# Kernel optimization log

Hardware: AMD Instinct MI355X
Metric: run time of the kernel (lower is better)

Reference implementation:

```python
import jax, jax.numpy as jnp
import numpy as np

B, L, D_MODEL = 4, 2048, 256
D_STATE, D_CONV, EXPAND = 16, 4, 2
D_INNER = EXPAND * D_MODEL          # 512
DT_RANK = (D_MODEL + 15) // 16      # 16
HORIZON = 96


def setup_inputs() -> dict:
    key = jax.random.key(0)
    ks = jax.random.split(key, 8)
    s = lambda k, shape, scale=0.02: jax.random.normal(k, shape, dtype=jnp.float32) * scale
    return {
        "x": jax.random.normal(ks[0], (B, L, D_MODEL), dtype=jnp.float32),
        "in_proj_w": s(ks[1], (2 * D_INNER, D_MODEL)),          # no bias (mamba default)
        "conv_w": s(ks[2], (D_INNER, 1, D_CONV), 0.1),          # depthwise causal conv
        "conv_b": jnp.zeros((D_INNER,), jnp.float32),
        "x_proj_w": s(ks[3], (DT_RANK + 2 * D_STATE, D_INNER)),
        "dt_proj_w": s(ks[4], (D_INNER, DT_RANK), 0.1),
        # softplus^{-1}(0.01): typical small initial dt
        "dt_proj_b": jnp.log(jnp.expm1(jnp.full((D_INNER,), 0.01, jnp.float32))),
        "A_log": jnp.log(jnp.broadcast_to(jnp.arange(1, D_STATE + 1, dtype=jnp.float32), (D_INNER, D_STATE))),
        "D_param": jnp.ones((D_INNER,), jnp.float32),
        "out_proj_w": s(ks[5], (D_MODEL, D_INNER)),
        "head_w": s(ks[6], (HORIZON, D_MODEL)),
        "head_b": jnp.zeros((HORIZON,), jnp.float32),
    }


def _silu(x):
    return x * jax.nn.sigmoid(x)


def _forward(x, in_proj_w, conv_w, conv_b, x_proj_w, dt_proj_w, dt_proj_b,
             A_log, D_param, out_proj_w, head_w, head_b):
    # in_proj -> split into conv/ssm branch and gate z
    xz = x @ in_proj_w.T                      # (B, L, 2*d_inner)
    x_in, z = jnp.split(xz, 2, axis=-1)
    # depthwise causal conv over time
    x_t = jnp.transpose(x_in, (0, 2, 1))      # (B, d_inner, L)
    x_conv = jax.lax.conv_general_dilated(
        x_t, conv_w, (1,), [(D_CONV - 1, 0)],
        feature_group_count=D_INNER, dimension_numbers=("NCH", "OIH", "NCH"))
    u = _silu(jnp.transpose(x_conv + conv_b[None, :, None], (0, 2, 1)))  # (B, L, d_inner)
    # input-dependent dt, B, C
    x_dbl = u @ x_proj_w.T
    dt, Bm, Cm = jnp.split(x_dbl, [DT_RANK, DT_RANK + D_STATE], axis=-1)
    delta = jax.nn.softplus(dt @ dt_proj_w.T + dt_proj_b)  # (B, L, d_inner)
    A = -jnp.exp(A_log)                                     # (d_inner, d_state)
    deltaA = jnp.exp(delta[..., None] * A)                  # (B, L, d_inner, d_state)
    deltaBu = delta[..., None] * Bm[:, :, None, :] * u[..., None]

    def step(h, ins):
        dA, dBu, c = ins                                    # (B,d,n),(B,d,n),(B,n)
        h = dA * h + dBu
        y = jnp.einsum("bdn,bn->bd", h, c)
        return h, y

    h0 = jnp.zeros((x.shape[0], D_INNER, D_STATE), x.dtype)
    xs = (jnp.moveaxis(deltaA, 1, 0), jnp.moveaxis(deltaBu, 1, 0), jnp.moveaxis(Cm, 1, 0))
    _, ys = jax.lax.scan(step, h0, xs)                      # (L, B, d_inner)
    y = jnp.moveaxis(ys, 0, 1) + u * D_param
    y = y * _silu(z)
    out = y @ out_proj_w.T                                  # (B, L, d_model)
    last = out[:, -1, :]
    return last @ head_w.T + head_b                         # (B, HORIZON)


def reference(x, in_proj_w, conv_w, conv_b, x_proj_w, dt_proj_w, dt_proj_b,
              A_log, D_param, out_proj_w, head_w, head_b):
    return _forward(x, in_proj_w, conv_w, conv_b, x_proj_w, dt_proj_w, dt_proj_b,
                    A_log, D_param, out_proj_w, head_w, head_b)
```

## Files before the change

kernel.cpp:

```cpp
#include <hip/hip_runtime.h>
#include <math.h>

#define BATCH 4
#define LSEQ 2048
#define BL (BATCH*LSEQ)
#define DMODEL 256
#define DINNER 512
#define NSTATE 16
#define DTRANK 16
#define NPROJ 48
#define HORIZ 96
#define NCH 32
#define TCH (LSEQ/NCH)
#define PSTRIDE (BL*NPROJ)

typedef __attribute__((ext_vector_type(8))) short short8b;
typedef __attribute__((ext_vector_type(4))) float f32x4;

__device__ __forceinline__ unsigned short f2bf(float f) {
  unsigned u = __float_as_uint(f);
  u += 0x7FFF + ((u >> 16) & 1);
  return (unsigned short)(u >> 16);
}

__global__ __launch_bounds__(512) void k_front(const float* __restrict__ X,
                                               const float* __restrict__ W,
                                               const float* __restrict__ cw,
                                               const float* __restrict__ cb,
                                               const float* __restrict__ xpw,
                                               const float* __restrict__ opw,
                                               const float* __restrict__ hw,
                                               float* __restrict__ uT,
                                               float* __restrict__ part,
                                               float* __restrict__ hwf) {
  __shared__ unsigned short sBX[48 * 264];
  __shared__ float sw2[48 * 132];
  __shared__ float u_lds[128 * 36];
  const int tid = threadIdx.x;
  const int bx = blockIdx.x;
  if (bx >= 512) {
    const int fid = bx - 512;
    const int k0 = fid * 8;
    float* scratch = u_lds;
    {
      int m = tid >> 1;
      int half = (tid & 1) << 2;
      *(float4*)&scratch[m * 8 + half] =
        *(const float4*)&opw[(size_t)m * DINNER + k0 + half];
    }
    __syncthreads();
    for (int u = tid; u < HORIZ * 8; u += 512) {
      int t = u >> 3, kk = u & 7;
      const float* hr = &hw[(size_t)t * DMODEL];
      float acc = 0.f;
      #pragma unroll 8
      for (int m = 0; m < DMODEL; ++m) acc = fmaf(hr[m], scratch[m*8 + kk], acc);
      hwf[(size_t)t * DINNER + k0 + kk] = acc;
    }
    return;
  }
  const int btc = bx >> 1;
  const int jp  = bx & 1;
  const int bt0 = btc * 32;
  const bool edge0 = ((bt0 & (LSEQ - 1)) == 0);
  const int lane = tid & 63;
  const int w  = tid >> 6;
  const int fl = lane & 15;
  const int fg = lane >> 4;
  for (int u = tid; u < 1536; u += 512) {
    int tok = u >> 5, ko = u & 31;
    int g = bt0 - 16 + tok;
    if (g < 0) g = 0;
    const float* xr = &X[(size_t)g * DMODEL + ko * 8];
    float4 a = *(const float4*)xr, b = *(const float4*)(xr + 4);
    unsigned short t8[8] = {f2bf(a.x), f2bf(a.y), f2bf(a.z), f2bf(a.w),
                            f2bf(b.x), f2bf(b.y), f2bf(b.z), f2bf(b.w)};
    *(short8b*)&sBX[tok * 264 + ko * 8] = *(short8b*)t8;
  }
  const int sj = tid >> 2;
  const int sk = tid & 3;
  const int tf = w & 1;
  const int of = w >> 1;
  f32x4 xacc = {0.f, 0.f, 0.f, 0.f};
  for (int jc = 0; jc < 2; ++jc) {
    const int jbase = jp * 256 + jc * 128;
    __syncthreads();
    for (int u = tid; u < 1536; u += 512) {
      int o = u >> 5, k4 = (u & 31) << 2;
      *(float4*)&sw2[o * 132 + k4] = *(const float4*)&xpw[(size_t)o * DINNER + jbase + k4];
    }
    short8b aw[8];
    {
      const float* wrow = &W[(size_t)(jbase + w * 16 + fl) * DMODEL + fg * 8];
      #pragma unroll
      for (int ks = 0; ks < 8; ++ks) {
        float4 a = *(const float4*)(wrow + ks * 32);
        float4 b = *(const float4*)(wrow + ks * 32 + 4);
        unsigned short t8[8] = {f2bf(a.x), f2bf(a.y), f2bf(a.z), f2bf(a.w),
                                f2bf(b.x), f2bf(b.y), f2bf(b.z), f2bf(b.w)};
        aw[ks] = *(short8b*)t8;
      }
    }
    f32x4 acc0 = {0,0,0,0}, acc1 = {0,0,0,0}, acc2 = {0,0,0,0};
    #pragma unroll
    for (int ks = 0; ks < 8; ++ks) {
      const int kcol = (ks * 4 + fg) * 8;
      short8b x0 = *(short8b*)&sBX[(fl)      * 264 + kcol];
      short8b x1 = *(short8b*)&sBX[(16 + fl) * 264 + kcol];
      short8b x2 = *(short8b*)&sBX[(32 + fl) * 264 + kcol];
      acc0 = __builtin_amdgcn_mfma_f32_16x16x32_bf16(x0, aw[ks], acc0, 0, 0, 0);
      acc1 = __builtin_amdgcn_mfma_f32_16x16x32_bf16(x1, aw[ks], acc1, 0, 0, 0);
      acc2 = __builtin_amdgcn_mfma_f32_16x16x32_bf16(x2, aw[ks], acc2, 0, 0, 0);
    }
    if (edge0) acc0 = (f32x4){0,0,0,0};
    const int j = jbase + w * 16 + fl;
    const float4 cwv = *(const float4*)&cw[j * 4];
    const float cbv = cb[j];
    float u1[4], u2[4];
    {
      float s3a = __shfl(acc1[3], lane - 16), s3b = __shfl(acc0[3], lane + 48);
      float s2a = __shfl(acc1[2], lane - 16), s2b = __shfl(acc0[2], lane + 48);
      float s1a = __shfl(acc1[1], lane - 16), s1b = __shfl(acc0[1], lane + 48);
      float p1 = fg ? s3a : s3b, p2 = fg ? s2a : s2b, p3 = fg ? s1a : s1b;
      float xm1[4] = {p1, acc1[0], acc1[1], acc1[2]};
      float xm2[4] = {p2, p1, acc1[0], acc1[1]};
      float xm3[4] = {p3, p2, p1, acc1[0]};
      #pragma unroll
      for (int r = 0; r < 4; ++r) {
        float s = cbv;
        s = fmaf(cwv.x, xm3[r], s); s = fmaf(cwv.y, xm2[r], s);
        s = fmaf(cwv.z, xm1[r], s); s = fmaf(cwv.w, acc1[r], s);
        u1[r] = s / (1.f + __expf(-s));
      }
    }
    {
      float s3a = __shfl(acc2[3], lane - 16), s3b = __shfl(acc1[3], lane + 48);
      float s2a = __shfl(acc2[2], lane - 16), s2b = __shfl(acc1[2], lane + 48);
      float s1a = __shfl(acc2[1], lane - 16), s1b = __shfl(acc1[1], lane + 48);
      float p1 = fg ? s3a : s3b, p2 = fg ? s2a : s2b, p3 = fg ? s1a : s1b;
      float xm1[4] = {p1, acc2[0], acc2[1], acc2[2]};
      float xm2[4] = {p2, p1, acc2[0], acc2[1]};
      float xm3[4] = {p3, p2, p1, acc2[0]};
      #pragma unroll
      for (int r = 0; r < 4; ++r) {
        float s = cbv;
        s = fmaf(cwv.x, xm3[r], s); s = fmaf(cwv.y, xm2[r], s);
        s = fmaf(cwv.z, xm1[r], s); s = fmaf(cwv.w, acc2[r], s);
        u2[r] = s / (1.f + __expf(-s));
      }
    }
    {
      const int jl = w * 16 + fl;
      #pragma unroll
      for (int r = 0; r < 4; ++r) {
        u_lds[jl * 36 + fg * 4 + r]      = u1[r];
        u_lds[jl * 36 + 16 + fg * 4 + r] = u2[r];
      }
    }
    __syncthreads();
    {
      const int tq = sk * 8;
      float4 a = *(float4*)&u_lds[sj * 36 + tq];
      float4 b = *(float4*)&u_lds[sj * 36 + tq + 4];
      *(float4*)&uT[(size_t)(jbase + sj) * BL + bt0 + tq]     = a;
      *(float4*)&uT[(size_t)(jbase + sj) * BL + bt0 + tq + 4] = b;
    }
    if (w < 6) {
      #pragma unroll
      for (int s = 0; s < 4; ++s) {
        unsigned short ua[8];
        #pragma unroll
        for (int e = 0; e < 8; ++e)
          ua[e] = f2bf(u_lds[(s * 32 + fg * 8 + e) * 36 + tf * 16 + fl]);
        const float* wr = &sw2[(of * 16 + fl) * 132 + s * 32 + fg * 8];
        float4 w0 = *(const float4*)wr, w1 = *(const float4*)(wr + 4);
        unsigned short wb[8] = {f2bf(w0.x), f2bf(w0.y), f2bf(w0.z), f2bf(w0.w),
                                f2bf(w1.x), f2bf(w1.y), f2bf(w1.z), f2bf(w1.w)};
        xacc = __builtin_amdgcn_mfma_f32_16x16x32_bf16(*(short8b*)ua, *(short8b*)wb,
                                                       xacc, 0, 0, 0);
      }
    }
  }
  if (w < 6) {
    float4 v = make_float4(xacc[0], xacc[1], xacc[2], xacc[3]);
    *(float4*)&part[(size_t)jp * PSTRIDE +
                    (size_t)(bt0 + tf * 16 + fl) * NPROJ + of * 16 + fg * 4] = v;
  }
}

__global__ __launch_bounds__(256) void k_scan(const float* __restrict__ uT,
                                              const float* __restrict__ part,
                                              const float* __restrict__ dtw,
                                              const float* __restrict__ dtb,
                                              const float* __restrict__ Alog,
                                              float* __restrict__ aprod,
                                              float* __restrict__ hacc) {
  __shared__ float sdt[64][17];
  __shared__ float sB[64][16];
  __shared__ float sdp[16][66][2];
  __shared__ float su[16][68];
  __shared__ float sdtw[16][17];
  __shared__ float sdtb[16];
  const int dblk = blockIdx.x, c = blockIdx.y, b = blockIdx.z;
  const int tid = threadIdx.x;
  const int d0 = dblk * 16;
  const int bt0 = b * LSEQ + c * TCH;
  {
    int tok = tid >> 2, q = (tid & 3) << 2;
    size_t base = (size_t)(bt0 + tok) * NPROJ + q;
    float4 v0 = *(const float4*)&part[base];
    float4 v1 = *(const float4*)&part[base + PSTRIDE];
    sdt[tok][q] = v0.x + v1.x; sdt[tok][q + 1] = v0.y + v1.y;
    sdt[tok][q + 2] = v0.z + v1.z; sdt[tok][q + 3] = v0.w + v1.w;
    float4 w0 = *(const float4*)&part[base + DTRANK];
    float4 w1 = *(const float4*)&part[base + DTRANK + PSTRIDE];
    float4 ww = make_float4(w0.x + w1.x, w0.y + w1.y, w0.z + w1.z, w0.w + w1.w);
    *(float4*)&sB[tok][q] = ww;
    int dl = tid >> 4, tq = (tid & 15) << 2;
    *(float4*)&su[dl][tq] = *(const float4*)&uT[(size_t)(d0 + dl) * BL + bt0 + tq];
    sdtw[tid >> 4][tid & 15] = dtw[(d0 + (tid >> 4)) * DTRANK + (tid & 15)];
    if (tid < 16) sdtb[tid] = dtb[d0 + tid];
  }
  __syncthreads();
  {
    int tok = tid >> 2, dl4 = (tid & 3) << 2;
    #pragma unroll
    for (int dd = 0; dd < 4; ++dd) {
      int dl = dl4 + dd;
      float a = sdtb[dl];
      #pragma unroll
      for (int r = 0; r < DTRANK; ++r) a = fmaf(sdt[tok][r], sdtw[dl][r], a);
      float dlt = (a > 20.f) ? a : log1pf(__expf(a));
      sdp[dl][tok][0] = dlt;
      sdp[dl][tok][1] = dlt * su[dl][tok];
    }
  }
  __syncthreads();
  const int dl = tid >> 4, n = tid & 15;
  const int d = d0 + dl;
  const float A = -__expf(Alog[d * NSTATE + n]);
  float ap = 1.f, h = 0.f;
  #pragma unroll 8
  for (int tt = 0; tt < TCH; ++tt) {
    float2 dp = *(const float2*)&sdp[dl][tt][0];
    float dA = __expf(dp.x * A);
    h = fmaf(dA, h, dp.y * sB[tt][n]);
    ap *= dA;
  }
  size_t off = (((size_t)b * NCH + c) * DINNER + d) * NSTATE + n;
  aprod[off] = ap;
  hacc[off] = h;
}

__global__ __launch_bounds__(256) void k_combine(const float* __restrict__ aprod,
                                                 const float* __restrict__ hacc,
                                                 const float* __restrict__ part,
                                                 const float* __restrict__ uT,
                                                 const float* __restrict__ Dp,
                                                 const float* __restrict__ X,
                                                 const float* __restrict__ ipw,
                                                 float* __restrict__ ybuf) {
  __shared__ float sx[DMODEL];
  const int dblk = blockIdx.x & 31, b = blockIdx.x >> 5;
  const int tid = threadIdx.x;
  const int dl = tid >> 4, n = tid & 15;
  const int d = dblk * 16 + dl;
  sx[tid] = X[((size_t)b * LSEQ + LSEQ - 1) * DMODEL + tid];
  float h = 0.f;
  for (int c = 0; c < NCH; ++c) {
    size_t off = (((size_t)b * NCH + c) * DINNER + d) * NSTATE + n;
    h = fmaf(aprod[off], h, hacc[off]);
  }
  __syncthreads();
  float zp = 0.f;
  {
    const float* zr = &ipw[(size_t)(DINNER + d) * DMODEL + (n << 4)];
    #pragma unroll
    for (int q = 0; q < 4; ++q) {
      float4 w4 = *(const float4*)&zr[q << 2];
      float4 x4 = *(const float4*)&sx[(n << 4) + (q << 2)];
      zp = fmaf(w4.x, x4.x, zp); zp = fmaf(w4.y, x4.y, zp);
      zp = fmaf(w4.z, x4.z, zp); zp = fmaf(w4.w, x4.w, zp);
    }
  }
  const int btL = b * LSEQ + LSEQ - 1;
  size_t cbase = (size_t)btL * NPROJ + DTRANK + NSTATE + n;
  float Cv = part[cbase] + part[cbase + PSTRIDE];
  float v = h * Cv;
  #pragma unroll
  for (int off = 1; off < 16; off <<= 1) {
    v  += __shfl_xor(v, off);
    zp += __shfl_xor(zp, off);
  }
  if (n == 0) {
    float y = v + uT[(size_t)d * BL + btL] * Dp[d];
    ybuf[b * DINNER + d] = y * zp / (1.f + __expf(-zp));
  }
}

__global__ __launch_bounds__(256) void k_out(const float* __restrict__ sy,
                                             const float* __restrict__ hwf,
                                             const float* __restrict__ hb,
                                             float* __restrict__ out) {
  const int t = blockIdx.x;
  const int b = threadIdx.x >> 6;
  const int lane = threadIdx.x & 63;
  const int k0 = lane << 3;
  const float* yr = &sy[(size_t)b * DINNER + k0];
  const float* wr = &hwf[(size_t)t * DINNER + k0];
  float4 y0 = *(const float4*)yr, y1 = *(const float4*)(yr + 4);
  float4 w0 = *(const float4*)wr, w1 = *(const float4*)(wr + 4);
  float s = y0.x * w0.x + y0.y * w0.y + y0.z * w0.z + y0.w * w0.w
          + y1.x * w1.x + y1.y * w1.y + y1.z * w1.z + y1.w * w1.w;
  #pragma unroll
  for (int off = 1; off < 64; off <<= 1) s += __shfl_xor(s, off);
  if (lane == 0) out[b * HORIZ + t] = s + hb[t];
}

extern "C" void kernel_launch(void* const* d_in, const int* in_sizes, int n_in,
                              void* d_out, int out_size, void* d_ws, size_t ws_size,
                              hipStream_t stream) {
  (void)in_sizes; (void)n_in; (void)out_size; (void)ws_size;
  const float* x    = (const float*)d_in[0];
  const float* ipw  = (const float*)d_in[1];
  const float* cw   = (const float*)d_in[2];
  const float* cb   = (const float*)d_in[3];
  const float* xpw  = (const float*)d_in[4];
  const float* dtw  = (const float*)d_in[5];
  const float* dtb  = (const float*)d_in[6];
  const float* Alog = (const float*)d_in[7];
  const float* Dp   = (const float*)d_in[8];
  const float* opw  = (const float*)d_in[9];
  const float* hw   = (const float*)d_in[10];
  const float* hb   = (const float*)d_in[11];
  float* out = (float*)d_out;
  float* ws  = (float*)d_ws;

  float* uT    = ws;
  float* part  = ws + 4194304;
  float* aprod = ws + 4980736;
  float* hacc  = ws + 6029312;
  float* ybuf  = ws + 7077888;
  float* hwf   = ws + 7079936;

  k_front<<<576, 512, 0, stream>>>(x, ipw, cw, cb, xpw, opw, hw, uT, part, hwf);
  k_scan<<<dim3(32, NCH, BATCH), 256, 0, stream>>>(uT, part, dtw, dtb, Alog, aprod, hacc);
  k_combine<<<128, 256, 0, stream>>>(aprod, hacc, part, uT, Dp, x, ipw, ybuf);
  k_out<<<HORIZ, 256, 0, stream>>>(ybuf, hwf, hb, out);
}
```

Before: 74.37 us.

## Store intermediate u activations in bf16 and pre-convert x_proj weights in LDS

New measurement: 72.55 us (median of 3 runs). -2.4%, faster.

```diff
diff --git a/kernel.cpp b/kernel.cpp
--- a/kernel.cpp
+++ b/kernel.cpp
@@ -15,12 +15,16 @@
 #define PSTRIDE (BL*NPROJ)
 
 typedef __attribute__((ext_vector_type(8))) short short8b;
+typedef __attribute__((ext_vector_type(4))) short short4b;
 typedef __attribute__((ext_vector_type(4))) float f32x4;
 
 __device__ __forceinline__ unsigned short f2bf(float f) {
   unsigned u = __float_as_uint(f);
   u += 0x7FFF + ((u >> 16) & 1);
   return (unsigned short)(u >> 16);
+}
+__device__ __forceinline__ float bf2f(unsigned short h) {
+  return __uint_as_float(((unsigned)h) << 16);
 }
 
 __global__ __launch_bounds__(512) void k_front(const float* __restrict__ X,
@@ -30,18 +34,18 @@
                                                const float* __restrict__ xpw,
                                                const float* __restrict__ opw,
                                                const float* __restrict__ hw,
-                                               float* __restrict__ uT,
+                                               unsigned short* __restrict__ uTb,
                                                float* __restrict__ part,
                                                float* __restrict__ hwf) {
   __shared__ unsigned short sBX[48 * 264];
-  __shared__ float sw2[48 * 132];
-  __shared__ float u_lds[128 * 36];
+  __shared__ unsigned short sw2b[48 * 136];
+  __shared__ unsigned short u_ldsb[128 * 40];
   const int tid = threadIdx.x;
   const int bx = blockIdx.x;
   if (bx >= 512) {
     const int fid = bx - 512;
     const int k0 = fid * 8;
-    float* scratch = u_lds;
+    float* scratch = (float*)sBX;
     {
       int m = tid >> 1;
       int half = (tid & 1) << 2;
@@ -59,8 +63,8 @@
     }
     return;
   }
-  const int btc = bx >> 1;
-  const int jp  = bx & 1;
+  const int btc = bx & 255;
+  const int jp  = bx >> 8;
   const int bt0 = btc * 32;
   const bool edge0 = ((bt0 & (LSEQ - 1)) == 0);
   const int lane = tid & 63;
@@ -85,9 +89,13 @@
   for (int jc = 0; jc < 2; ++jc) {
     const int jbase = jp * 256 + jc * 128;
     __syncthreads();
-    for (int u = tid; u < 1536; u += 512) {
-      int o = u >> 5, k4 = (u & 31) << 2;
-      *(float4*)&sw2[o * 132 + k4] = *(const float4*)&xpw[(size_t)o * DINNER + jbase + k4];
+    for (int u = tid; u < 768; u += 512) {
+      int o = u >> 4, k8 = (u & 15) * 8;
+      const float* src = &xpw[(size_t)o * DINNER + jbase + k8];
+      float4 a = *(const float4*)src, b = *(const float4*)(src + 4);
+      unsigned short t8[8] = {f2bf(a.x), f2bf(a.y), f2bf(a.z), f2bf(a.w),
+                              f2bf(b.x), f2bf(b.y), f2bf(b.z), f2bf(b.w)};
+      *(short8b*)&sw2b[o * 136 + k8] = *(short8b*)t8;
     }
     short8b aw[8];
     {
@@ -151,19 +159,16 @@
     }
     {
       const int jl = w * 16 + fl;
-      #pragma unroll
-      for (int r = 0; r < 4; ++r) {
-        u_lds[jl * 36 + fg * 4 + r]      = u1[r];
-        u_lds[jl * 36 + 16 + fg * 4 + r] = u2[r];
-      }
+      unsigned short b1[4] = {f2bf(u1[0]), f2bf(u1[1]), f2bf(u1[2]), f2bf(u1[3])};
+      unsigned short b2[4] = {f2bf(u2[0]), f2bf(u2[1]), f2bf(u2[2]), f2bf(u2[3])};
+      *(short4b*)&u_ldsb[jl * 40 + fg * 4]      = *(short4b*)b1;
+      *(short4b*)&u_ldsb[jl * 40 + 16 + fg * 4] = *(short4b*)b2;
     }
     __syncthreads();
     {
       const int tq = sk * 8;
-      float4 a = *(float4*)&u_lds[sj * 36 + tq];
-      float4 b = *(float4*)&u_lds[sj * 36 + tq + 4];
-      *(float4*)&uT[(size_t)(jbase + sj) * BL + bt0 + tq]     = a;
-      *(float4*)&uT[(size_t)(jbase + sj) * BL + bt0 + tq + 4] = b;
+      *(short8b*)&uTb[(size_t)(jbase + sj) * BL + bt0 + tq] =
+        *(short8b*)&u_ldsb[sj * 40 + tq];
     }
     if (w < 6) {
       #pragma unroll
@@ -171,12 +176,9 @@
         unsigned short ua[8];
         #pragma unroll
         for (int e = 0; e < 8; ++e)
-          ua[e] = f2bf(u_lds[(s * 32 + fg * 8 + e) * 36 + tf * 16 + fl]);
-        const float* wr = &sw2[(of * 16 + fl) * 132 + s * 32 + fg * 8];
-        float4 w0 = *(const float4*)wr, w1 = *(const float4*)(wr + 4);
-        unsigned short wb[8] = {f2bf(w0.x), f2bf(w0.y), f2bf(w0.z), f2bf(w0.w),
-                                f2bf(w1.x), f2bf(w1.y), f2bf(w1.z), f2bf(w1.w)};
-        xacc = __builtin_amdgcn_mfma_f32_16x16x32_bf16(*(short8b*)ua, *(short8b*)wb,
+          ua[e] = u_ldsb[(s * 32 + fg * 8 + e) * 40 + tf * 16 + fl];
+        short8b wb = *(short8b*)&sw2b[(of * 16 + fl) * 136 + s * 32 + fg * 8];
+        xacc = __builtin_amdgcn_mfma_f32_16x16x32_bf16(*(short8b*)ua, wb,
                                                        xacc, 0, 0, 0);
       }
     }
@@ -188,7 +190,7 @@
   }
 }
 
-__global__ __launch_bounds__(256) void k_scan(const float* __restrict__ uT,
+__global__ __launch_bounds__(256) void k_scan(const unsigned short* __restrict__ uTb,
                                               const float* __restrict__ part,
                                               const float* __restrict__ dtw,
                                               const float* __restrict__ dtb,
@@ -216,8 +218,12 @@
     float4 w1 = *(const float4*)&part[base + DTRANK + PSTRIDE];
     float4 ww = make_float4(w0.x + w1.x, w0.y + w1.y, w0.z + w1.z, w0.w + w1.w);
     *(float4*)&sB[tok][q] = ww;
-    int dl = tid >> 4, tq = (tid & 15) << 2;
-    *(float4*)&su[dl][tq] = *(const float4*)&uT[(size_t)(d0 + dl) * BL + bt0 + tq];
+    int dl = tid >> 4, t4 = (tid & 15) << 2;
+    short4b uv = *(const short4b*)&uTb[(size_t)(d0 + dl) * BL + bt0 + t4];
+    su[dl][t4 + 0] = bf2f((unsigned short)uv[0]);
+    su[dl][t4 + 1] = bf2f((unsigned short)uv[1]);
+    su[dl][t4 + 2] = bf2f((unsigned short)uv[2]);
+    su[dl][t4 + 3] = bf2f((unsigned short)uv[3]);
     sdtw[tid >> 4][tid & 15] = dtw[(d0 + (tid >> 4)) * DTRANK + (tid & 15)];
     if (tid < 16) sdtb[tid] = dtb[d0 + tid];
   }
@@ -255,7 +261,7 @@
 __global__ __launch_bounds__(256) void k_combine(const float* __restrict__ aprod,
                                                  const float* __restrict__ hacc,
                                                  const float* __restrict__ part,
-                                                 const float* __restrict__ uT,
+                                                 const unsigned short* __restrict__ uTb,
                                                  const float* __restrict__ Dp,
                                                  const float* __restrict__ X,
                                                  const float* __restrict__ ipw,
@@ -293,7 +299,7 @@
     zp += __shfl_xor(zp, off);
   }
   if (n == 0) {
-    float y = v + uT[(size_t)d * BL + btL] * Dp[d];
+    float y = v + bf2f(uTb[(size_t)d * BL + btL]) * Dp[d];
     ybuf[b * DINNER + d] = y * zp / (1.f + __expf(-zp));
   }
 }
@@ -336,15 +342,15 @@
   float* out = (float*)d_out;
   float* ws  = (float*)d_ws;
 
-  float* uT    = ws;
-  float* part  = ws + 4194304;
-  float* aprod = ws + 4980736;
-  float* hacc  = ws + 6029312;
-  float* ybuf  = ws + 7077888;
-  float* hwf   = ws + 7079936;
-
-  k_front<<<576, 512, 0, stream>>>(x, ipw, cw, cb, xpw, opw, hw, uT, part, hwf);
-  k_scan<<<dim3(32, NCH, BATCH), 256, 0, stream>>>(uT, part, dtw, dtb, Alog, aprod, hacc);
-  k_combine<<<128, 256, 0, stream>>>(aprod, hacc, part, uT, Dp, x, ipw, ybuf);
+  unsigned short* uTb = (unsigned short*)ws;
+  float* part  = ws + 2097152;
+  float* aprod = ws + 2883584;
+  float* hacc  = ws + 3932160;
+  float* ybuf  = ws + 4980736;
+  float* hwf   = ws + 4982784;
+
+  k_front<<<576, 512, 0, stream>>>(x, ipw, cw, cb, xpw, opw, hw, uTb, part, hwf);
+  k_scan<<<dim3(32, NCH, BATCH), 256, 0, stream>>>(uTb, part, dtw, dtb, Alog, aprod, hacc);
+  k_combine<<<128, 256, 0, stream>>>(aprod, hacc, part, uTb, Dp, x, ipw, ybuf);
   k_out<<<HORIZ, 256, 0, stream>>>(ybuf, hwf, hb, out);
 }
```
